# Performance work log

Hardware: AMD Instinct MI355X
Metric: run time of the kernel (lower is better)

Reference implementation:

```python
import jax, jax.numpy as jnp
import numpy as np

# config constants (from init_kwargs)
IMG_W = 800
IMG_H = 320
NUM_POINTS = 72
N_STRIPS = NUM_POINTS - 1
MAX_LANES = 4
REFINE_LAYERS = 3
CLS_W, REG_W, IOU_W = 2.0, 0.5, 2.0
ALPHA_NEG, ALPHA_POS, GAMMA = 0.1, 0.9, 2.0
LIOU_LEN = 15.0


def setup_inputs() -> dict:
    key = jax.random.key(0)
    k1, k2, k3, k4 = jax.random.split(key, 4)
    S, B, N, L, D = REFINE_LAYERS, 32, 2000, MAX_LANES, 2 + 4 + NUM_POINTS
    pred_fir = jax.random.uniform(k1, (S, B, N, D), dtype=jnp.float32)
    pred_sec = jax.random.uniform(k2, (S, B, N, D), dtype=jnp.float32)
    gt = jax.random.uniform(k3, (B, L, D), dtype=jnp.float32)
    gt = gt.at[..., 1].set(1.0)                    # all lanes valid
    # target offsets live in pixel coords; let some fall outside [0, IMG_W) to exercise invalid mask
    gt = gt.at[..., 6:].set(gt[..., 6:] * (IMG_W * 1.1) - 0.05 * IMG_W)
    diff = jax.random.uniform(k4, (S, N), dtype=jnp.float32)
    return {"predictions_fir": pred_fir, "predictions_sec": pred_sec,
            "gt_lane": gt, "diff": diff}


def _greedy_assign(cost):
    # cost: [N, L] -> matched prior row per target column, greedy without replacement
    N = cost.shape[0]
    def body(used, col):
        c = jnp.where(used, jnp.inf, col)
        r = jnp.argmin(c)
        return used.at[r].set(True), r
    _, rows = jax.lax.scan(body, jnp.zeros((N,), bool), cost.T)
    return rows  # [L] int32


def _assign_all(preds, gt):
    # preds: [S,B,N,D], gt: [B,L,D]; matching is under no_grad in the original
    p = jax.lax.stop_gradient(preds)
    t = jax.lax.stop_gradient(gt)
    score = jax.nn.softmax(p[..., :2], axis=-1)[..., 1]            # [S,B,N]
    geo = jnp.abs(p[..., :, None, 2:6] - t[None, :, None, :, 2:6]).sum(-1)   # [S,B,N,L]
    off = jnp.abs(p[..., :, None, 6:] - t[None, :, None, :, 6:] / (IMG_W - 1)).mean(-1)
    cost = geo + off - score[..., None]                            # [S,B,N,L]
    S, B, N, L = cost.shape
    rows = jax.vmap(_greedy_assign)(cost.reshape(S * B, N, L))
    return rows.reshape(S, B, L)


def _smooth_l1(d):
    ad = jnp.abs(d)
    return jnp.where(ad < 1.0, 0.5 * d * d, ad - 0.5)


def _branch_loss(preds, gt):
    # preds: [S,B,N,D], gt: [B,L,D] -> instance loss [N], last matched rows [L]
    S, B, N, _ = preds.shape
    L = gt.shape[1]
    rows = _assign_all(preds, gt)                                  # [S,B,L]

    # focal cls loss, per prior, summed over stages & batch
    cls_t = jax.nn.one_hot(rows, N, dtype=preds.dtype).sum(2)      # [S,B,N] 0/1
    logp = jax.nn.log_softmax(preds[..., :2], axis=-1)
    logpt = jnp.where(cls_t > 0, logp[..., 1], logp[..., 0])
    pt = jnp.exp(logpt)
    alpha_t = jnp.where(cls_t > 0, ALPHA_POS, ALPHA_NEG)
    cls_loss = (-alpha_t * (1.0 - pt) ** GAMMA * logpt).sum((0, 1)) / (B * REFINE_LAYERS)  # [N]

    # gather matched priors: [S,B,L,D]
    pm = jnp.take_along_axis(preds, rows[..., None], axis=2)
    tgt = gt[None]                                                 # [1,B,L,D]

    # smooth-L1 on (y, x, theta, length)
    sc = jnp.array([N_STRIPS, IMG_W - 1, 180.0, N_STRIPS], preds.dtype)
    d = pm[..., 2:6] * sc - tgt[..., 2:6] * sc
    reg_loss = (_smooth_l1(d).mean(-1) / L).sum((0, 1)) / (B * REFINE_LAYERS)  # [L]

    # line IoU loss on offsets
    rp = pm[..., 6:] * (IMG_W - 1)
    rt = jnp.broadcast_to(tgt[..., 6:], rp.shape)
    invalid = (rt < 0) | (rt >= IMG_W)
    ovr = jnp.minimum(rp + LIOU_LEN, rt + LIOU_LEN) - jnp.maximum(rp - LIOU_LEN, rt - LIOU_LEN)
    uni = jnp.maximum(rp + LIOU_LEN, rt + LIOU_LEN) - jnp.minimum(rp - LIOU_LEN, rt - LIOU_LEN)
    ovr = jnp.where(invalid, 0.0, ovr)
    uni = jnp.where(invalid, 0.0, uni)
    iou = ovr.sum(-1) / (uni.sum(-1) + 1e-9)                       # [S,B,L]
    iou_loss = ((1.0 - iou) / L).sum((0, 1)) / (B * REFINE_LAYERS) # [L]

    inst = cls_loss * CLS_W
    rows_last = rows[-1, -1]                                       # last stage, last image
    inst = inst.at[rows_last].add(reg_loss * REG_W + iou_loss * IOU_W)
    return inst


def reference(predictions_fir, predictions_sec, gt_lane, diff):
    loss_A = _branch_loss(predictions_fir, gt_lane)   # [N]
    loss_B = _branch_loss(predictions_sec, gt_lane)   # [N]
    diff_mean = diff.mean(0)                          # [N]
    delta = jax.lax.stop_gradient(jnp.median(loss_A - loss_B))
    loss_A = loss_A - delta / 2
    loss_B = loss_B + delta / 2
    total = jnp.sum((1.0 - diff_mean) * loss_A + diff_mean * loss_B)
    return total
```

## Files before the change

kernel.cpp:

```cpp
#include <hip/hip_runtime.h>
#include <math.h>

#define SDIM 3
#define BDIM 32
#define NPRI 2000
#define LDIM 4
#define DDIM 78
#define NSB (SDIM * BDIM)


__global__ __launch_bounds__(1024) void fused_kernel(
    const float* __restrict__ predsA, const float* __restrict__ predsB,
    const float* __restrict__ gt,
    int* __restrict__ rowsws, float* __restrict__ regacc,
    float* __restrict__ corrws, float* __restrict__ clsSum)
{
    const int sb = blockIdx.x, branch = blockIdx.y;
    const float* preds = branch ? predsB : predsA;
    const int bimg = sb % BDIM;
    const int tid = threadIdx.x;
    const int wv = tid >> 6, lane = tid & 63;

    __shared__ float cost[LDIM][NPRI];
    __shared__ float tg[36 * 8];
    __shared__ float geo4[16];
    __shared__ float redv[16];
    __shared__ int   redi[16];
    __shared__ int   rows_lds[LDIM];

    {
        const float* gtb = gt + (size_t)bimg * LDIM * DDIM;
        if (tid < 288) {
            int jj = tid >> 3, t = tid & 7, l = t >> 1, k = t & 1;
            tg[tid] = gtb[l * DDIM + 6 + 2 * jj + k] / 799.0f;
        }
        if (tid < 16) geo4[tid] = gtb[(tid >> 2) * DDIM + 2 + (tid & 3)];
    }
    __syncthreads();

    const int h = tid & 3;
    const float* gpb = preds + (size_t)sb * NPRI * DDIM;

    for (int pass = 0; pass < 8; ++pass) {
        const int n = pass * 256 + (tid >> 2);
        if (n < NPRI) {
            const float* p = gpb + (size_t)n * DDIM;
            float2 hd0 = *(const float2*)(p);
            float2 hd1 = *(const float2*)(p + 2);
            float2 hd2 = *(const float2*)(p + 4);
            const float2* pb = (const float2*)(p + 6 + h * 18);
            float2 ov[9];
#pragma unroll
            for (int q = 0; q < 9; ++q) ov[q] = pb[q];

            float offs0 = 0.f, offs1 = 0.f, offs2 = 0.f, offs3 = 0.f;
#pragma unroll
            for (int q = 0; q < 9; ++q) {
                float pv0 = ov[q].x;
                float pv1 = ov[q].y;
                const float4* t4 = (const float4*)(tg + (h * 9 + q) * 8);
                float4 ta = t4[0], tb = t4[1];
                offs0 += fabsf(pv0 - ta.x); offs0 += fabsf(pv1 - ta.y);
                offs1 += fabsf(pv0 - ta.z); offs1 += fabsf(pv1 - ta.w);
                offs2 += fabsf(pv0 - tb.x); offs2 += fabsf(pv1 - tb.y);
                offs3 += fabsf(pv0 - tb.z); offs3 += fabsf(pv1 - tb.w);
            }
            offs0 += __shfl_xor(offs0, 1); offs1 += __shfl_xor(offs1, 1);
            offs2 += __shfl_xor(offs2, 1); offs3 += __shfl_xor(offs3, 1);
            offs0 += __shfl_xor(offs0, 2); offs1 += __shfl_xor(offs1, 2);
            offs2 += __shfl_xor(offs2, 2); offs3 += __shfl_xor(offs3, 2);

            float a = hd0.x, b1 = hd0.y;
            float m = fmaxf(a, b1);
            float ea = expf(a - m), eb = expf(b1 - m);
            float score = eb / (ea + eb);
            float g0 = hd1.x, g1 = hd1.y, g2 = hd2.x, g3 = hd2.y;

            float mo01 = (h & 1) ? offs1 : offs0;
            float mo23 = (h & 1) ? offs3 : offs2;
            float myoffs = (h & 2) ? mo23 : mo01;

            float geo = fabsf(g0 - geo4[h * 4 + 0]) + fabsf(g1 - geo4[h * 4 + 1])
                      + fabsf(g2 - geo4[h * 4 + 2]) + fabsf(g3 - geo4[h * 4 + 3]);
            cost[h][n] = geo + myoffs / 72.0f - score;

            if (h == 0) {
                float lse = m + logf(ea + eb);
                float logpt = a - lse;
                float pt = expf(logpt);
                float om = 1.0f - pt;
                atomicAdd(&clsSum[branch * NPRI + n], -(0.1f * om * om * logpt));
            }
        }
    }
    __syncthreads();

    for (int l = 0; l < LDIM; ++l) {
        float bv = INFINITY; int bi = 0x7fffffff;
        for (int k = tid; k < NPRI; k += 1024) {
            float v = cost[l][k];
            if (v < bv) { bv = v; bi = k; }
        }
#pragma unroll
        for (int off = 32; off > 0; off >>= 1) {
            float v2 = __shfl_down(bv, off);
            int   i2 = __shfl_down(bi, off);
            if (v2 < bv || (v2 == bv && i2 < bi)) { bv = v2; bi = i2; }
        }
        if (lane == 0) { redv[wv] = bv; redi[wv] = bi; }
        __syncthreads();
        if (tid == 0) {
            float fv = redv[0]; int fi = redi[0];
#pragma unroll
            for (int w = 1; w < 16; ++w)
                if (redv[w] < fv || (redv[w] == fv && redi[w] < fi)) { fv = redv[w]; fi = redi[w]; }
            rows_lds[l] = fi;
            cost[0][fi] = INFINITY; cost[1][fi] = INFINITY;
            cost[2][fi] = INFINITY; cost[3][fi] = INFINITY;
        }
        __syncthreads();
    }
    if (tid < LDIM && sb == NSB - 1) rowsws[branch * LDIM + tid] = rows_lds[tid];

    if (wv < 4) {
        const int l = wv;
        const int row = rows_lds[l];
        const float* pm = preds + ((size_t)sb * NPRI + row) * DDIM;
        const float* tgp = gt + ((size_t)bimg * LDIM + l) * DDIM;

        float osum = 0.f, usum = 0.f, rterm = 0.f;
        {
            float rp = pm[6 + lane] * 799.0f;
            float rt = tgp[6 + lane];
            bool inv = (rt < 0.0f) || (rt >= 800.0f);
            float ov = fminf(rp, rt) - fmaxf(rp, rt) + 30.0f;
            float un = fmaxf(rp, rt) - fminf(rp, rt) + 30.0f;
            if (!inv) { osum += ov; usum += un; }
        }
        if (lane < 8) {
            float rp = pm[6 + lane + 64] * 799.0f;
            float rt = tgp[6 + lane + 64];
            bool inv = (rt < 0.0f) || (rt >= 800.0f);
            float ov = fminf(rp, rt) - fmaxf(rp, rt) + 30.0f;
            float un = fmaxf(rp, rt) - fminf(rp, rt) + 30.0f;
            if (!inv) { osum += ov; usum += un; }
        }
        if (lane < 4) {
            const float scv[4] = {71.0f, 799.0f, 180.0f, 71.0f};
            float s = scv[lane];
            float d = pm[2 + lane] * s - tgp[2 + lane] * s;
            float ad = fabsf(d);
            rterm = (ad < 1.0f) ? 0.5f * d * d : ad - 0.5f;
        }
#pragma unroll
        for (int off = 32; off > 0; off >>= 1) {
            osum += __shfl_down(osum, off);
            usum += __shfl_down(usum, off);
            rterm += __shfl_down(rterm, off);
        }
        if (lane == 0) {
            float iou = osum / (usum + 1e-9f);
            atomicAdd(&regacc[branch * 8 + l], (rterm / 4.0f) / 4.0f);
            atomicAdd(&regacc[branch * 8 + 4 + l], (1.0f - iou) / 4.0f);

            float a = pm[0], b1 = pm[1];
            float m = fmaxf(a, b1);
            float ea = expf(a - m), eb = expf(b1 - m);
            float lse = m + logf(ea + eb);
            float lp0 = a - lse, lp1 = b1 - lse;
            float pt0 = expf(lp0), pt1 = expf(lp1);
            float om0 = 1.0f - pt0, om1 = 1.0f - pt1;
            float neg = -(0.1f * om0 * om0 * lp0);
            float pos = -(0.9f * om1 * om1 * lp1);
            atomicAdd(&corrws[branch * NPRI + row], pos - neg);
        }
    }
}

__device__ __forceinline__ unsigned mapf(float f) {
    unsigned u = __float_as_uint(f);
    return (u & 0x80000000u) ? ~u : (u | 0x80000000u);
}
__device__ __forceinline__ float unmapf(unsigned u) {
    return (u & 0x80000000u) ? __uint_as_float(u ^ 0x80000000u)
                             : __uint_as_float(~u);
}

__global__ __launch_bounds__(1024) void final_kernel(
    const float* __restrict__ clsSum, const float* __restrict__ corrws,
    const float* __restrict__ regacc, const int* __restrict__ rowsws,
    const float* __restrict__ diff, float* __restrict__ out)
{
    __shared__ float instA[NPRI];
    __shared__ float instB[NPRI];
    __shared__ unsigned keys[NPRI];
    __shared__ unsigned bufA[NPRI];
    __shared__ unsigned bufB[NPRI];
    __shared__ unsigned cnt[256];
    __shared__ unsigned wpre[4];
    __shared__ unsigned selBin, selBefore, outCnt;
    __shared__ int      redc[16];
    __shared__ unsigned redm[16];
    __shared__ float    deltaSh;
    __shared__ float    red[1024];
    const int tid = threadIdx.x;
    const int wv = tid >> 6, lane = tid & 63;

    for (int n = tid; n < NPRI; n += 1024) {
        float ia = (clsSum[n] + corrws[n]) * (2.0f / 96.0f);
        float ib = (clsSum[NPRI + n] + corrws[NPRI + n]) * (2.0f / 96.0f);
#pragma unroll
        for (int l = 0; l < 4; ++l) {
            if (rowsws[l] == n)
                ia += (regacc[l] / 96.0f) * 0.5f + (regacc[4 + l] / 96.0f) * 2.0f;
            if (rowsws[4 + l] == n)
                ib += (regacc[8 + l] / 96.0f) * 0.5f + (regacc[12 + l] / 96.0f) * 2.0f;
        }
        instA[n] = ia; instB[n] = ib;
        keys[n] = mapf(ia - ib);
    }
    __syncthreads();

    int curk = 999;
    unsigned prefix = 0;
    unsigned m = NPRI;
    unsigned* src = keys;
    unsigned* dst = bufA;

    for (int r = 0; r < 4; ++r) {
        const int shift = 24 - 8 * r;
        if (tid < 256) cnt[tid] = 0;
        __syncthreads();
        for (unsigned i = tid; i < m; i += 1024)
            atomicAdd(&cnt[(src[i] >> shift) & 255u], 1u);
        __syncthreads();

        unsigned v = 0, inc = 0;
        if (tid < 256) {
            v = cnt[tid]; inc = v;
#pragma unroll
            for (int o = 1; o < 64; o <<= 1) {
                unsigned t = __shfl_up(inc, o);
                if ((tid & 63) >= o) inc += t;
            }
            if ((tid & 63) == 63) wpre[tid >> 6] = inc;
        }
        __syncthreads();
        if (tid < 256) {
            unsigned base = 0;
#pragma unroll
            for (int w = 0; w < 3; ++w) if (w < (tid >> 6)) base += wpre[w];
            unsigned incl = base + inc, excl = incl - v;
            if (v > 0 && (unsigned)curk >= excl && (unsigned)curk < incl) {
                selBin = tid; selBefore = excl;
            }
        }
        __syncthreads();
        const unsigned b = selBin;
        curk -= (int)selBefore;
        prefix |= b << shift;

        if (r < 3) {
            if (tid == 0) outCnt = 0;
            __syncthreads();
            for (unsigned i = tid; i < m; i += 1024) {
                unsigned u = src[i];
                if (((u >> shift) & 255u) == b) {
                    unsigned p = atomicAdd(&outCnt, 1u);
                    dst[p] = u;
                }
            }
            __syncthreads();
            m = outCnt;
            src = dst;
            dst = (dst == bufA) ? bufB : bufA;
        }
    }
    const unsigned v999u = prefix;

    {
        int cle = 0; unsigned mn = 0xffffffffu;
        for (int j = tid; j < NPRI; j += 1024) {
            unsigned u = keys[j];
            cle += (u <= v999u);
            if (u > v999u) mn = min(mn, u);
        }
#pragma unroll
        for (int off = 32; off > 0; off >>= 1) {
            cle += __shfl_down(cle, off);
            mn = min(mn, (unsigned)__shfl_down(mn, off));
        }
        if (lane == 0) { redc[wv] = cle; redm[wv] = mn; }
        __syncthreads();
        if (tid == 0) {
            int c = 0; unsigned m2 = 0xffffffffu;
#pragma unroll
            for (int w = 0; w < 16; ++w) { c += redc[w]; m2 = min(m2, redm[w]); }
            unsigned v1000u = (c >= 1001) ? v999u : m2;
            deltaSh = 0.5f * (unmapf(v999u) + unmapf(v1000u));
        }
        __syncthreads();
    }
    const float delta = deltaSh;

    float acc = 0.0f;
    for (int n = tid; n < NPRI; n += 1024) {
        float dm = (diff[n] + diff[NPRI + n] + diff[2 * NPRI + n]) / 3.0f;
        acc += (1.0f - dm) * (instA[n] - 0.5f * delta)
             + dm * (instB[n] + 0.5f * delta);
    }
    red[tid] = acc;
    __syncthreads();
    for (int s = 512; s > 0; s >>= 1) {
        if (tid < s) red[tid] += red[tid + s];
        __syncthreads();
    }
    if (tid == 0) out[0] = red[0];
}

extern "C" void kernel_launch(void* const* d_in, const int* in_sizes, int n_in,
                              void* d_out, int out_size, void* d_ws, size_t ws_size,
                              hipStream_t stream)
{
    const float* predsA = (const float*)d_in[0];
    const float* predsB = (const float*)d_in[1];
    const float* gt     = (const float*)d_in[2];
    const float* diff   = (const float*)d_in[3];
    float* out = (float*)d_out;

    int*   rowsws = (int*)d_ws;
    float* clsSum = (float*)(rowsws + 8);
    float* corrws = clsSum + 2 * NPRI;
    float* regacc = corrws + 2 * NPRI;

    hipMemsetAsync(clsSum, 0, (4 * NPRI + 16) * sizeof(float), stream);

    dim3 g1(NSB, 2);
    fused_kernel<<<g1, 1024, 0, stream>>>(predsA, predsB, gt,
                                          rowsws, regacc, corrws, clsSum);

    final_kernel<<<1, 1024, 0, stream>>>(clsSum, corrws, regacc, rowsws, diff, out);
}
```

Before: 170.8 us.

## Stage prediction tiles in LDS with coalesced float4 loads and register prefetch

Each pass now loads a 256-prior tile of predictions into shared memory using fully coalesced float4 loads. The cost computation then reads rows from LDS instead of issuing strided per-thread global float2 loads. The next tile is prefetched into registers while the current one is processed, double-buffering through registers so global latency overlaps compute. The change also adds a second launch-bounds argument. That argument may tighten register limits, and the roughly 80 KB tile adds to LDS use, which limits residency.

```diff
diff --git a/kernel.cpp b/kernel.cpp
--- a/kernel.cpp
+++ b/kernel.cpp
@@ -9,7 +9,7 @@
 #define NSB (SDIM * BDIM)
 
 
-__global__ __launch_bounds__(1024) void fused_kernel(
+__global__ __launch_bounds__(1024, 4) void fused_kernel(
     const float* __restrict__ predsA, const float* __restrict__ predsB,
     const float* __restrict__ gt,
     int* __restrict__ rowsws, float* __restrict__ regacc,
@@ -21,6 +21,7 @@
     const int tid = threadIdx.x;
     const int wv = tid >> 6, lane = tid & 63;
 
+    __shared__ __align__(16) float tile[256 * DDIM];
     __shared__ float cost[LDIM][NPRI];
     __shared__ float tg[36 * 8];
     __shared__ float geo4[16];
@@ -36,61 +37,98 @@
         }
         if (tid < 16) geo4[tid] = gtb[(tid >> 2) * DDIM + 2 + (tid & 3)];
     }
+
+    const int h = tid & 3;
+    const float4* gs4 = (const float4*)(preds + (size_t)sb * NPRI * DDIM);
+    float4* t4 = (float4*)tile;
+    float4 s0, s1, s2, s3, s4;
+
+    {
+        const float4* b = gs4;
+        s0 = b[tid]; s1 = b[tid + 1024]; s2 = b[tid + 2048]; s3 = b[tid + 3072];
+        if (tid < 896) s4 = b[tid + 4096];
+        t4[tid] = s0; t4[tid + 1024] = s1; t4[tid + 2048] = s2; t4[tid + 3072] = s3;
+        if (tid < 896) t4[tid + 4096] = s4;
+    }
     __syncthreads();
 
-    const int h = tid & 3;
-    const float* gpb = preds + (size_t)sb * NPRI * DDIM;
-
     for (int pass = 0; pass < 8; ++pass) {
-        const int n = pass * 256 + (tid >> 2);
-        if (n < NPRI) {
-            const float* p = gpb + (size_t)n * DDIM;
-            float2 hd0 = *(const float2*)(p);
-            float2 hd1 = *(const float2*)(p + 2);
-            float2 hd2 = *(const float2*)(p + 4);
-            const float2* pb = (const float2*)(p + 6 + h * 18);
-            float2 ov[9];
-#pragma unroll
-            for (int q = 0; q < 9; ++q) ov[q] = pb[q];
-
-            float offs0 = 0.f, offs1 = 0.f, offs2 = 0.f, offs3 = 0.f;
-#pragma unroll
-            for (int q = 0; q < 9; ++q) {
-                float pv0 = ov[q].x;
-                float pv1 = ov[q].y;
-                const float4* t4 = (const float4*)(tg + (h * 9 + q) * 8);
-                float4 ta = t4[0], tb = t4[1];
-                offs0 += fabsf(pv0 - ta.x); offs0 += fabsf(pv1 - ta.y);
-                offs1 += fabsf(pv0 - ta.z); offs1 += fabsf(pv1 - ta.w);
-                offs2 += fabsf(pv0 - tb.x); offs2 += fabsf(pv1 - tb.y);
-                offs3 += fabsf(pv0 - tb.z); offs3 += fabsf(pv1 - tb.w);
-            }
-            offs0 += __shfl_xor(offs0, 1); offs1 += __shfl_xor(offs1, 1);
-            offs2 += __shfl_xor(offs2, 1); offs3 += __shfl_xor(offs3, 1);
-            offs0 += __shfl_xor(offs0, 2); offs1 += __shfl_xor(offs1, 2);
-            offs2 += __shfl_xor(offs2, 2); offs3 += __shfl_xor(offs3, 2);
-
-            float a = hd0.x, b1 = hd0.y;
-            float m = fmaxf(a, b1);
-            float ea = expf(a - m), eb = expf(b1 - m);
-            float score = eb / (ea + eb);
-            float g0 = hd1.x, g1 = hd1.y, g2 = hd2.x, g3 = hd2.y;
-
-            float mo01 = (h & 1) ? offs1 : offs0;
-            float mo23 = (h & 1) ? offs3 : offs2;
-            float myoffs = (h & 2) ? mo23 : mo01;
-
-            float geo = fabsf(g0 - geo4[h * 4 + 0]) + fabsf(g1 - geo4[h * 4 + 1])
-                      + fabsf(g2 - geo4[h * 4 + 2]) + fabsf(g3 - geo4[h * 4 + 3]);
-            cost[h][n] = geo + myoffs / 72.0f - score;
-
-            if (h == 0) {
-                float lse = m + logf(ea + eb);
-                float logpt = a - lse;
-                float pt = expf(logpt);
-                float om = 1.0f - pt;
-                atomicAdd(&clsSum[branch * NPRI + n], -(0.1f * om * om * logpt));
-            }
+        const bool haveNext = (pass < 7);
+        const bool nextFull = (pass + 1 < 7);
+        if (haveNext) {
+            const float4* b = gs4 + (size_t)(pass + 1) * 4992;
+            s0 = b[tid]; s1 = b[tid + 1024]; s2 = b[tid + 2048];
+            if (nextFull) {
+                s3 = b[tid + 3072];
+                if (tid < 896) s4 = b[tid + 4096];
+            } else {
+                if (tid < 984) s3 = b[tid + 3072];
+            }
+        }
+
+        {
+            const int i = tid >> 2;
+            const int n = pass * 256 + i;
+            if (n < NPRI) {
+                const float* pr = &tile[i * DDIM];
+                float2 hd0 = *(const float2*)(pr);
+                float2 hd1 = *(const float2*)(pr + 2);
+                float2 hd2 = *(const float2*)(pr + 4);
+                const float2* pb = (const float2*)(pr + 6 + h * 18);
+                float2 ov[9];
+#pragma unroll
+                for (int q = 0; q < 9; ++q) ov[q] = pb[q];
+
+                float offs0 = 0.f, offs1 = 0.f, offs2 = 0.f, offs3 = 0.f;
+#pragma unroll
+                for (int q = 0; q < 9; ++q) {
+                    float pv0 = ov[q].x;
+                    float pv1 = ov[q].y;
+                    const float4* tt4 = (const float4*)(tg + (h * 9 + q) * 8);
+                    float4 ta = tt4[0], tb = tt4[1];
+                    offs0 += fabsf(pv0 - ta.x); offs0 += fabsf(pv1 - ta.y);
+                    offs1 += fabsf(pv0 - ta.z); offs1 += fabsf(pv1 - ta.w);
+                    offs2 += fabsf(pv0 - tb.x); offs2 += fabsf(pv1 - tb.y);
+                    offs3 += fabsf(pv0 - tb.z); offs3 += fabsf(pv1 - tb.w);
+                }
+                offs0 += __shfl_xor(offs0, 1); offs1 += __shfl_xor(offs1, 1);
+                offs2 += __shfl_xor(offs2, 1); offs3 += __shfl_xor(offs3, 1);
+                offs0 += __shfl_xor(offs0, 2); offs1 += __shfl_xor(offs1, 2);
+                offs2 += __shfl_xor(offs2, 2); offs3 += __shfl_xor(offs3, 2);
+
+                float a = hd0.x, b1 = hd0.y;
+                float m = fmaxf(a, b1);
+                float ea = expf(a - m), eb = expf(b1 - m);
+                float score = eb / (ea + eb);
+                float g0 = hd1.x, g1 = hd1.y, g2 = hd2.x, g3 = hd2.y;
+
+                float mo01 = (h & 1) ? offs1 : offs0;
+                float mo23 = (h & 1) ? offs3 : offs2;
+                float myoffs = (h & 2) ? mo23 : mo01;
+
+                float geo = fabsf(g0 - geo4[h * 4 + 0]) + fabsf(g1 - geo4[h * 4 + 1])
+                          + fabsf(g2 - geo4[h * 4 + 2]) + fabsf(g3 - geo4[h * 4 + 3]);
+                cost[h][n] = geo + myoffs / 72.0f - score;
+
+                if (h == 0) {
+                    float lse = m + logf(ea + eb);
+                    float logpt = a - lse;
+                    float pt = expf(logpt);
+                    float om = 1.0f - pt;
+                    atomicAdd(&clsSum[branch * NPRI + n], -(0.1f * om * om * logpt));
+                }
+            }
+        }
+        __syncthreads();
+        if (haveNext) {
+            t4[tid] = s0; t4[tid + 1024] = s1; t4[tid + 2048] = s2;
+            if (nextFull) {
+                t4[tid + 3072] = s3;
+                if (tid < 896) t4[tid + 4096] = s4;
+            } else {
+                if (tid < 984) t4[tid + 3072] = s3;
+            }
+            __syncthreads();
         }
     }
     __syncthreads();
```

Result: faster. 165.7 us (-3.0%).
